# Kernel tuning notes

Hardware: AMD Instinct MI355X
Metric: run time of the kernel (lower is better)

The kernel has to match this reference:

```python
import jax, jax.numpy as jnp
import numpy as np
import math

COV_WEIGHT = 1.0
BANDWIDTH_FACTOR = 1.06
SQRT_2PI = math.sqrt(2.0 * math.pi)
EPS_LOG = 1e-8
H_MIN = 1e-4


def setup_inputs() -> dict:
    key = jax.random.key(0)
    activity = jax.random.normal(key, (2048, 64), dtype=jnp.float32)
    return {"activity": activity}


def reference(activity):
    B, R = activity.shape
    # Silverman bandwidth per receptor (torch .std uses ddof=1)
    std = jnp.std(activity, axis=0, ddof=1)                     # (R,)
    h = jnp.maximum(BANDWIDTH_FACTOR * std * (B ** (-0.2)), H_MIN)  # (R,)

    # Pairwise Gaussian KDE: query == samples == activity
    u = (activity[:, None, :] - activity[None, :, :]) / h       # (B_q, B_s, R)
    kernel_values = jnp.exp(-0.5 * u * u) / SQRT_2PI             # (B_q, B_s, R)
    density = kernel_values.sum(axis=1) / (B * h)                # (B_q, R)

    entropies = -jnp.mean(jnp.log(density + EPS_LOG), axis=0)    # (R,)
    loss_entropy = -entropies.mean()

    # Covariance penalty: sum of squared off-diagonals
    centered = activity - activity.mean(axis=0, keepdims=True)
    cov = (centered.T @ centered) / (B - 1)                      # (R, R)
    off = cov - jnp.diag(jnp.diag(cov))
    loss_cov = jnp.sum(off * off)

    total_loss = loss_entropy + COV_WEIGHT * loss_cov
    return total_loss
```

## Files before the change

kernel.cpp:

```cpp
#include <hip/hip_runtime.h>
#include <math.h>

#define B_SZ 2048
#define R_SZ 64
#define QT 8
#define KDE_BLOCKS (B_SZ / QT)

#define B_POW_NEG02 0.217637640824031f
#define SQRT_2PI 2.5066282746310002f
#define LOG2E 1.44269504088896340736f

extern "C" __device__ float __ocml_native_exp2_f32(float);

typedef __attribute__((ext_vector_type(2))) float f32x2;


__global__ __launch_bounds__(1024) void cov_stats_kernel(const float* __restrict__ A,
                                                         float* __restrict__ U,
                                                         float* __restrict__ lscale,
                                                         float* __restrict__ cov_partial,
                                                         float* __restrict__ ent_acc,
                                                         int* __restrict__ done_cnt) {
    int i = blockIdx.x;
    int tid = threadIdx.x;
    int j = tid & 63, bg = tid >> 6;

    float g = 0.f, sj = 0.f, s2j = 0.f;
#pragma unroll 4
    for (int b = bg; b < B_SZ; b += 16) {
        float ai = A[b * R_SZ + i];
        float aj = A[b * R_SZ + j];
        g = fmaf(ai, aj, g);
        sj += aj;
        s2j = fmaf(aj, aj, s2j);
    }

    __shared__ float gred[16][64], sred[16][64], s2red[16][64];
    __shared__ float gfin[64], sfin[64], hs[64];
    gred[bg][j] = g; sred[bg][j] = sj; s2red[bg][j] = s2j;
    __syncthreads();
    if (tid < 64) {
        float G = 0.f, S = 0.f, S2 = 0.f;
#pragma unroll
        for (int t = 0; t < 16; ++t) { G += gred[t][j]; S += sred[t][j]; S2 += s2red[t][j]; }
        gfin[j] = G;
        sfin[j] = S;
        float m = S * (1.f / (float)B_SZ);
        float var = (S2 - S * m) * (1.f / (float)(B_SZ - 1));
        var = fmaxf(var, 0.f);
        float h = fmaxf(1.06f * sqrtf(var) * B_POW_NEG02, 1e-4f);
        hs[j] = sqrtf(0.5f * LOG2E) / h;
        if (i == 0) lscale[j] = 1.0f / ((float)B_SZ * h * SQRT_2PI);
    }
    __syncthreads();
    if (tid < 64) {
        float m_j = sfin[j] * (1.f / (float)B_SZ);
        float m_i = sfin[i] * (1.f / (float)B_SZ);
        float cov = (gfin[j] - (float)B_SZ * m_i * m_j) * (1.f / (float)(B_SZ - 1));
        float v = (j == i) ? 0.f : cov * cov;
        for (int off = 32; off > 0; off >>= 1) v += __shfl_down(v, off, 64);
        if (j == 0) cov_partial[i] = v;
    }
    if (i == 0 && tid == 64) { *ent_acc = 0.f; *done_cnt = 0; }

    int base = i * (32 * R_SZ);
    float k0 = hs[tid & 63];
    U[base + tid]        = A[base + tid]        * k0;
    U[base + 1024 + tid] = A[base + 1024 + tid] * k0;
}

__global__ __launch_bounds__(1024) void kde_kernel(const float* __restrict__ U,
                                                   const float* __restrict__ lscale,
                                                   const float* __restrict__ cov_partial,
                                                   float* __restrict__ ent_acc,
                                                   int* __restrict__ done_cnt,
                                                   float* __restrict__ out) {
    int tid = threadIdx.x;
    int r = tid & 63, sg = tid >> 6;
    int q0 = blockIdx.x * QT;

    f32x2 uq01 = { U[(q0 + 0) * R_SZ + r], U[(q0 + 1) * R_SZ + r] };
    f32x2 uq23 = { U[(q0 + 2) * R_SZ + r], U[(q0 + 3) * R_SZ + r] };
    f32x2 uq45 = { U[(q0 + 4) * R_SZ + r], U[(q0 + 5) * R_SZ + r] };
    f32x2 uq67 = { U[(q0 + 6) * R_SZ + r], U[(q0 + 7) * R_SZ + r] };
    f32x2 c01 = { 0.f, 0.f }, c23 = { 0.f, 0.f };
    f32x2 c45 = { 0.f, 0.f }, c67 = { 0.f, 0.f };

#define KDE_BODY(usv)                                                          \
    {                                                                          \
        f32x2 uss = { (usv), (usv) };                                          \
        f32x2 d01 = uq01 - uss, d23 = uq23 - uss;                              \
        f32x2 d45 = uq45 - uss, d67 = uq67 - uss;                              \
        f32x2 n01 = -d01 * d01, n23 = -d23 * d23;                              \
        f32x2 n45 = -d45 * d45, n67 = -d67 * d67;                              \
        f32x2 e01 = { __ocml_native_exp2_f32(n01.x), __ocml_native_exp2_f32(n01.y) }; \
        f32x2 e23 = { __ocml_native_exp2_f32(n23.x), __ocml_native_exp2_f32(n23.y) }; \
        f32x2 e45 = { __ocml_native_exp2_f32(n45.x), __ocml_native_exp2_f32(n45.y) }; \
        f32x2 e67 = { __ocml_native_exp2_f32(n67.x), __ocml_native_exp2_f32(n67.y) }; \
        c01 += e01; c23 += e23; c45 += e45; c67 += e67;                        \
    }

    const float* Up = U + sg * R_SZ + r;
    float p[8];
#pragma unroll
    for (int j = 0; j < 8; ++j) p[j] = Up[j * 1024];

    int li = 8 * 1024;
#pragma unroll 1
    for (int k = 0; k < 15; ++k) {
#pragma unroll
        for (int j = 0; j < 8; ++j) {
            float us = p[j];
            p[j] = Up[li + j * 1024];
            KDE_BODY(us);
        }
        li += 8 * 1024;
    }
#pragma unroll
    for (int j = 0; j < 8; ++j) KDE_BODY(p[j]);

#undef KDE_BODY

    __shared__ float red[16][QT][64];
    red[sg][0][r] = c01.x; red[sg][1][r] = c01.y;
    red[sg][2][r] = c23.x; red[sg][3][r] = c23.y;
    red[sg][4][r] = c45.x; red[sg][5][r] = c45.y;
    red[sg][6][r] = c67.x; red[sg][7][r] = c67.y;
    __syncthreads();
    __shared__ float wred[QT];
    if (sg < QT) {
        float S = 0.f;
#pragma unroll
        for (int t = 0; t < 16; ++t) S += red[t][sg][r];
        float v = __logf(fmaf(S, lscale[r], 1e-8f));
        for (int off = 32; off > 0; off >>= 1) v += __shfl_down(v, off, 64);
        if (r == 0) wred[sg] = v;
    }
    __syncthreads();
    __shared__ int lastflag;
    if (tid == 0) {
        float p2 = 0.f;
#pragma unroll
        for (int t = 0; t < QT; ++t) p2 += wred[t];
        p2 *= (1.0f / ((float)B_SZ * (float)R_SZ));
        atomicAdd(ent_acc, p2);
        __threadfence();
        int prev = atomicAdd(done_cnt, 1);
        lastflag = (prev == KDE_BLOCKS - 1);
    }
    __syncthreads();
    if (lastflag && tid < 64) {
        __threadfence();
        float v = cov_partial[tid];
        for (int off = 32; off > 0; off >>= 1) v += __shfl_down(v, off, 64);
        if (tid == 0) {
            float ent = __hip_atomic_load(ent_acc, __ATOMIC_ACQUIRE,
                                          __HIP_MEMORY_SCOPE_AGENT);
            out[0] = ent + v;
        }
    }
}

extern "C" void kernel_launch(void* const* d_in, const int* in_sizes, int n_in,
                              void* d_out, int out_size, void* d_ws, size_t ws_size,
                              hipStream_t stream) {
    const float* A = (const float*)d_in[0];
    float* out = (float*)d_out;

    float* wsf = (float*)d_ws;
    float* lscale      = wsf;
    float* cov_partial = wsf + 64;
    float* ent_acc     = wsf + 160;
    int*   done_cnt    = (int*)(wsf + 192);
    float* U           = wsf + 256;

    cov_stats_kernel<<<R_SZ, 1024, 0, stream>>>(A, U, lscale, cov_partial,
                                                ent_acc, done_cnt);
    kde_kernel<<<KDE_BLOCKS, 1024, 0, stream>>>(U, lscale, cov_partial,
                                                ent_acc, done_cnt, out);
}
```

Baseline: 100.4 us.

## Split stats/gram pass into quarter-batch blocks and fold scaling into KDE kernel

The first kernel now runs 256 blocks, each covering a quarter of the batch for one receptor row, and writes only partial sums and partial Gram rows. The bandwidth computation and scaling of activations move into the KDE kernel, so the pre-scaled U buffer is no longer written or read. The final covariance penalty is computed by the last KDE block from the partial Gram matrix. In exchange, every KDE block recomputes the per-receptor stats and does an extra multiply per sample inside the hot loop, and the last block does a larger reduction.

After: 95.84 us. 4.6% less time.

```diff
diff --git a/kernel.cpp b/kernel.cpp
--- a/kernel.cpp
+++ b/kernel.cpp
@@ -15,74 +15,74 @@
 typedef __attribute__((ext_vector_type(2))) float f32x2;
 
 
-__global__ __launch_bounds__(1024) void cov_stats_kernel(const float* __restrict__ A,
-                                                         float* __restrict__ U,
-                                                         float* __restrict__ lscale,
-                                                         float* __restrict__ cov_partial,
-                                                         float* __restrict__ ent_acc,
-                                                         int* __restrict__ done_cnt) {
-    int i = blockIdx.x;
+__global__ __launch_bounds__(1024) void stats_gram_kernel(const float* __restrict__ A,
+                                                          float* __restrict__ qsums,
+                                                          float* __restrict__ qsums2,
+                                                          float* __restrict__ gram4,
+                                                          float* __restrict__ ent_acc,
+                                                          int* __restrict__ done_cnt) {
+    int b = blockIdx.x;
+    int i = b >> 2, qd = b & 3;
     int tid = threadIdx.x;
     int j = tid & 63, bg = tid >> 6;
 
+    const float* __restrict__ Aq = A + (qd * 512) * R_SZ;
     float g = 0.f, sj = 0.f, s2j = 0.f;
 #pragma unroll 4
-    for (int b = bg; b < B_SZ; b += 16) {
-        float ai = A[b * R_SZ + i];
-        float aj = A[b * R_SZ + j];
+    for (int t = bg; t < 512; t += 16) {
+        float ai = Aq[t * R_SZ + i];
+        float aj = Aq[t * R_SZ + j];
         g = fmaf(ai, aj, g);
         sj += aj;
         s2j = fmaf(aj, aj, s2j);
     }
 
     __shared__ float gred[16][64], sred[16][64], s2red[16][64];
-    __shared__ float gfin[64], sfin[64], hs[64];
     gred[bg][j] = g; sred[bg][j] = sj; s2red[bg][j] = s2j;
     __syncthreads();
     if (tid < 64) {
         float G = 0.f, S = 0.f, S2 = 0.f;
 #pragma unroll
         for (int t = 0; t < 16; ++t) { G += gred[t][j]; S += sred[t][j]; S2 += s2red[t][j]; }
-        gfin[j] = G;
-        sfin[j] = S;
-        float m = S * (1.f / (float)B_SZ);
-        float var = (S2 - S * m) * (1.f / (float)(B_SZ - 1));
-        var = fmaxf(var, 0.f);
-        float h = fmaxf(1.06f * sqrtf(var) * B_POW_NEG02, 1e-4f);
-        hs[j] = sqrtf(0.5f * LOG2E) / h;
-        if (i == 0) lscale[j] = 1.0f / ((float)B_SZ * h * SQRT_2PI);
+        gram4[b * 64 + j] = G;
+        if (i == 0) {
+            qsums[qd * 64 + j]  = S;
+            qsums2[qd * 64 + j] = S2;
+        }
     }
-    __syncthreads();
-    if (tid < 64) {
-        float m_j = sfin[j] * (1.f / (float)B_SZ);
-        float m_i = sfin[i] * (1.f / (float)B_SZ);
-        float cov = (gfin[j] - (float)B_SZ * m_i * m_j) * (1.f / (float)(B_SZ - 1));
-        float v = (j == i) ? 0.f : cov * cov;
-        for (int off = 32; off > 0; off >>= 1) v += __shfl_down(v, off, 64);
-        if (j == 0) cov_partial[i] = v;
-    }
-    if (i == 0 && tid == 64) { *ent_acc = 0.f; *done_cnt = 0; }
-
-    int base = i * (32 * R_SZ);
-    float k0 = hs[tid & 63];
-    U[base + tid]        = A[base + tid]        * k0;
-    U[base + 1024 + tid] = A[base + 1024 + tid] * k0;
+    if (b == 0 && tid == 64) { *ent_acc = 0.f; *done_cnt = 0; }
 }
 
-__global__ __launch_bounds__(1024) void kde_kernel(const float* __restrict__ U,
-                                                   const float* __restrict__ lscale,
-                                                   const float* __restrict__ cov_partial,
+__global__ __launch_bounds__(1024) void kde_kernel(const float* __restrict__ A,
+                                                   const float* __restrict__ qsums,
+                                                   const float* __restrict__ qsums2,
+                                                   const float* __restrict__ gram4,
                                                    float* __restrict__ ent_acc,
                                                    int* __restrict__ done_cnt,
                                                    float* __restrict__ out) {
     int tid = threadIdx.x;
     int r = tid & 63, sg = tid >> 6;
+
+    __shared__ float k0s[64], lscs[64], sums_s[64];
+    if (tid < 64) {
+        float S  = qsums[tid]  + qsums[64 + tid]  + qsums[128 + tid]  + qsums[192 + tid];
+        float S2 = qsums2[tid] + qsums2[64 + tid] + qsums2[128 + tid] + qsums2[192 + tid];
+        float m = S * (1.f / (float)B_SZ);
+        float var = (S2 - S * m) * (1.f / (float)(B_SZ - 1));
+        var = fmaxf(var, 0.f);
+        float h = fmaxf(1.06f * sqrtf(var) * B_POW_NEG02, 1e-4f);
+        k0s[tid]  = sqrtf(0.5f * LOG2E) / h;
+        lscs[tid] = 1.0f / ((float)B_SZ * h * SQRT_2PI);
+        sums_s[tid] = S;
+    }
+    __syncthreads();
+    float k0 = k0s[r];
+
     int q0 = blockIdx.x * QT;
-
-    f32x2 uq01 = { U[(q0 + 0) * R_SZ + r], U[(q0 + 1) * R_SZ + r] };
-    f32x2 uq23 = { U[(q0 + 2) * R_SZ + r], U[(q0 + 3) * R_SZ + r] };
-    f32x2 uq45 = { U[(q0 + 4) * R_SZ + r], U[(q0 + 5) * R_SZ + r] };
-    f32x2 uq67 = { U[(q0 + 6) * R_SZ + r], U[(q0 + 7) * R_SZ + r] };
+    f32x2 uq01 = { A[(q0 + 0) * R_SZ + r] * k0, A[(q0 + 1) * R_SZ + r] * k0 };
+    f32x2 uq23 = { A[(q0 + 2) * R_SZ + r] * k0, A[(q0 + 3) * R_SZ + r] * k0 };
+    f32x2 uq45 = { A[(q0 + 4) * R_SZ + r] * k0, A[(q0 + 5) * R_SZ + r] * k0 };
+    f32x2 uq67 = { A[(q0 + 6) * R_SZ + r] * k0, A[(q0 + 7) * R_SZ + r] * k0 };
     f32x2 c01 = { 0.f, 0.f }, c23 = { 0.f, 0.f };
     f32x2 c45 = { 0.f, 0.f }, c67 = { 0.f, 0.f };
 
@@ -100,24 +100,24 @@
         c01 += e01; c23 += e23; c45 += e45; c67 += e67;                        \
     }
 
-    const float* Up = U + sg * R_SZ + r;
+    const float* __restrict__ Ap = A + sg * R_SZ + r;
     float p[8];
 #pragma unroll
-    for (int j = 0; j < 8; ++j) p[j] = Up[j * 1024];
+    for (int j = 0; j < 8; ++j) p[j] = Ap[j * 1024];
 
     int li = 8 * 1024;
 #pragma unroll 1
     for (int k = 0; k < 15; ++k) {
 #pragma unroll
         for (int j = 0; j < 8; ++j) {
-            float us = p[j];
-            p[j] = Up[li + j * 1024];
+            float us = p[j] * k0;
+            p[j] = Ap[li + j * 1024];
             KDE_BODY(us);
         }
         li += 8 * 1024;
     }
 #pragma unroll
-    for (int j = 0; j < 8; ++j) KDE_BODY(p[j]);
+    for (int j = 0; j < 8; ++j) { float us = p[j] * k0; KDE_BODY(us); }
 
 #undef KDE_BODY
 
@@ -132,7 +132,7 @@
         float S = 0.f;
 #pragma unroll
         for (int t = 0; t < 16; ++t) S += red[t][sg][r];
-        float v = __logf(fmaf(S, lscale[r], 1e-8f));
+        float v = __logf(fmaf(S, lscs[r], 1e-8f));
         for (int off = 32; off > 0; off >>= 1) v += __shfl_down(v, off, 64);
         if (r == 0) wred[sg] = v;
     }
@@ -149,14 +149,30 @@
         lastflag = (prev == KDE_BLOCKS - 1);
     }
     __syncthreads();
-    if (lastflag && tid < 64) {
+    if (lastflag) {
         __threadfence();
-        float v = cov_partial[tid];
+        float v = 0.f;
+#pragma unroll
+        for (int c = tid; c < 4096; c += 1024) {
+            int ii = c >> 6, jj = c & 63;
+            const float* gp = gram4 + ii * 256 + jj;
+            float G = gp[0] + gp[64] + gp[128] + gp[192];
+            float mi = sums_s[ii] * (1.f / (float)B_SZ);
+            float mj = sums_s[jj] * (1.f / (float)B_SZ);
+            float cov = (G - (float)B_SZ * mi * mj) * (1.f / (float)(B_SZ - 1));
+            if (ii != jj) v = fmaf(cov, cov, v);
+        }
         for (int off = 32; off > 0; off >>= 1) v += __shfl_down(v, off, 64);
+        __shared__ float wsum[16];
+        if (r == 0) wsum[sg] = v;
+        __syncthreads();
         if (tid == 0) {
+            float C = 0.f;
+#pragma unroll
+            for (int t = 0; t < 16; ++t) C += wsum[t];
             float ent = __hip_atomic_load(ent_acc, __ATOMIC_ACQUIRE,
                                           __HIP_MEMORY_SCOPE_AGENT);
-            out[0] = ent + v;
+            out[0] = ent + C;
         }
     }
 }
@@ -168,14 +184,14 @@
     float* out = (float*)d_out;
 
     float* wsf = (float*)d_ws;
-    float* lscale      = wsf;
-    float* cov_partial = wsf + 64;
-    float* ent_acc     = wsf + 160;
-    int*   done_cnt    = (int*)(wsf + 192);
-    float* U           = wsf + 256;
+    float* qsums   = wsf;
+    float* qsums2  = wsf + 256;
+    float* ent_acc = wsf + 640;
+    int*   done_cnt = (int*)(wsf + 672);
+    float* gram4   = wsf + 1024;
 
-    cov_stats_kernel<<<R_SZ, 1024, 0, stream>>>(A, U, lscale, cov_partial,
+    stats_gram_kernel<<<256, 1024, 0, stream>>>(A, qsums, qsums2, gram4,
                                                 ent_acc, done_cnt);
-    kde_kernel<<<KDE_BLOCKS, 1024, 0, stream>>>(U, lscale, cov_partial,
+    kde_kernel<<<KDE_BLOCKS, 1024, 0, stream>>>(A, qsums, qsums2, gram4,
                                                 ent_acc, done_cnt, out);
 }
```
